# Kernel optimization log

Hardware: AMD Instinct MI355X
Metric: run time of the kernel (lower is better)

## Reference

```python
import jax, jax.numpy as jnp
import numpy as np
import math

B, S, E, H, DFF = 4, 1024, 1024, 16, 4096
HD = E // H
EPS = 1e-8


def setup_inputs() -> dict:
    key = jax.random.key(0)
    ks = jax.random.split(key, 16)
    sc = 0.02
    inp = {
        'x': jax.random.normal(ks[0], (B, S, E), jnp.float32),
        'mask': jax.random.randint(ks[1], (B, S, S), 0, 2, jnp.int32),
        'Wq': jax.random.normal(ks[2], (E, E), jnp.float32) * sc,
        'bq': jnp.zeros((E,), jnp.float32),
        'Wk': jax.random.normal(ks[3], (E, E), jnp.float32) * sc,
        'bk': jnp.zeros((E,), jnp.float32),
        'Wv': jax.random.normal(ks[4], (E, E), jnp.float32) * sc,
        'bv': jnp.zeros((E,), jnp.float32),
        'Wo': jax.random.normal(ks[5], (E, E), jnp.float32) * sc,
        'bo': jnp.zeros((E,), jnp.float32),
        'W1': jax.random.normal(ks[6], (DFF, E), jnp.float32) * sc,
        'b1': jnp.zeros((DFF,), jnp.float32),
        'W2': jax.random.normal(ks[7], (E, DFF), jnp.float32) * sc,
        'b2': jnp.zeros((E,), jnp.float32),
        'g1': jnp.ones((E,), jnp.float32),
        'be1': jnp.zeros((E,), jnp.float32),
        'g2': jnp.ones((E,), jnp.float32),
        'be2': jnp.zeros((E,), jnp.float32),
    }
    return inp


def _layernorm(x, g, b):
    # torch LayerNorm here: (x-mean)/(std+eps), std is unbiased (ddof=1)
    mean = jnp.mean(x, axis=-1, keepdims=True)
    std = jnp.std(x, axis=-1, keepdims=True, ddof=1)
    return g * (x - mean) / (std + EPS) + b


def _gelu(x):
    c = math.sqrt(2.0 / math.pi)
    return 0.5 * x * (1.0 + jnp.tanh(c * (x + 0.044715 * x ** 3)))


def _block(x, mask_f, Wq, bq, Wk, bk, Wv, bv, Wo, bo, W1, b1, W2, b2, g1, be1, g2, be2):
    # --- attention sublayer (pre-norm, residual) ---
    nx = _layernorm(x, g1, be1)
    q = (nx @ Wq.T + bq).reshape(B, S, H, HD).transpose(0, 2, 1, 3)  # [B,H,S,D]
    k = (nx @ Wk.T + bk).reshape(B, S, H, HD).transpose(0, 2, 1, 3)
    v = (nx @ Wv.T + bv).reshape(B, S, H, HD).transpose(0, 2, 1, 3)
    scores = jnp.einsum('bhqd,bhkd->bhqk', q, k) / math.sqrt(HD)
    m = mask_f[:, None, :, :]  # [B,1,S,S]
    scores = jnp.where(m == 0, jnp.float32(-0.01), scores * m)
    p = jax.nn.softmax(scores, axis=-1)
    o = jnp.einsum('bhqk,bhkd->bhqd', p, v)  # [B,H,S,D]
    o = o.transpose(0, 2, 1, 3).reshape(B, S, E)
    x = x + (o @ Wo.T + bo)
    # --- FFN sublayer ---
    nx2 = _layernorm(x, g2, be2)
    ff = _gelu(nx2 @ W1.T + b1) @ W2.T + b2
    return x + ff


def reference(x, mask, Wq, bq, Wk, bk, Wv, bv, Wo, bo, W1, b1, W2, b2, g1, be1, g2, be2):
    mask_f = mask.astype(jnp.float32)
    return _block(x, mask_f, Wq, bq, Wk, bk, Wv, bv, Wo, bo, W1, b1, W2, b2, g1, be1, g2, be2)
```

## Files before the change

### kernel.cpp

```cpp
#include <hip/hip_runtime.h>
#include <math.h>

typedef __attribute__((ext_vector_type(8))) short short8;
typedef __attribute__((ext_vector_type(4))) float f32x4;
typedef __attribute__((ext_vector_type(4))) int   i32x4v;

#define B_   4
#define S_   1024
#define E_   1024
#define H_   16
#define DFF_ 4096

#define HB_MAX 4.0f

__device__ __forceinline__ ushort f2bf(float f){
  unsigned int x = __float_as_uint(f);
  x += 0x7fffu + ((x >> 16) & 1u);
  return (ushort)(x >> 16);
}

__device__ __forceinline__ unsigned int pk_bf16_trunc(float a, float b){
  return __builtin_amdgcn_perm(__float_as_uint(b), __float_as_uint(a), 0x07060302u);
}

__device__ __forceinline__ float gelu_f(float x){
  const float c = 0.7978845608028654f;
  float u = 2.0f * c * (x + 0.044715f * x * x * x);
  return x / (1.0f + __expf(-u));
}

__device__ __forceinline__ void gl2lds16(const void* g, void* l){
  __builtin_amdgcn_global_load_lds(
      (const __attribute__((address_space(1))) void*)g,
      (__attribute__((address_space(3))) void*)l, 16, 0, 0);
}

__device__ __forceinline__ int q8(float x, float s){
  float v = fmaxf(fminf(x * s, 127.f), -127.f);
  return ((int)__builtin_rintf(v)) & 255;
}
__device__ __forceinline__ int pk_i8x4(float a, float b, float c, float d, float s){
  return q8(a,s) | (q8(b,s) << 8) | (q8(c,s) << 16) | (q8(d,s) << 24);
}

__global__ __launch_bounds__(256) void prep_kernel(
    const float* __restrict__ Wq, const float* __restrict__ Wk,
    const float* __restrict__ Wv, const float* __restrict__ Wo,
    const float* __restrict__ W1, const float* __restrict__ W2,
    const float* __restrict__ bq, const float* __restrict__ bk,
    const float* __restrict__ bv, const int* __restrict__ mask,
    unsigned char* __restrict__ bQKV8, float* __restrict__ sQKV,
    unsigned char* __restrict__ bWo8, float* __restrict__ sWo,
    unsigned char* __restrict__ bW18, float* __restrict__ sW1,
    unsigned char* __restrict__ bW28, float* __restrict__ sW2,
    float* __restrict__ cbias, unsigned long long* __restrict__ maskp)
{
  int blk = blockIdx.x, t = threadIdx.x;
  __shared__ float sm[4];

  if (blk < 4096){
    float4 v = ((const float4*)(W1 + (size_t)blk * 1024))[t];
    float m = fmaxf(fmaxf(fabsf(v.x), fabsf(v.y)), fmaxf(fabsf(v.z), fabsf(v.w)));
    #pragma unroll
    for (int o = 32; o; o >>= 1) m = fmaxf(m, __shfl_xor(m, o));
    if ((t & 63) == 0) sm[t >> 6] = m;
    __syncthreads();
    float mx = fmaxf(fmaxf(sm[0], sm[1]), fmaxf(sm[2], sm[3])) + 1e-20f;
    float qs = 127.0f / mx;
    ((int*)(bW18 + (size_t)blk * 1024))[t] = pk_i8x4(v.x, v.y, v.z, v.w, qs);
    if (t == 0) sW1[blk] = mx * (1.0f / 127.0f);
    return;
  }
  if (blk < 5120){
    int r = blk - 4096;
    float4 v[4]; float m = 0.f;
    #pragma unroll
    for (int i = 0; i < 4; i++){
      v[i] = ((const float4*)(W2 + (size_t)r * 4096))[t + i * 256];
      m = fmaxf(m, fmaxf(fmaxf(fabsf(v[i].x), fabsf(v[i].y)), fmaxf(fabsf(v[i].z), fabsf(v[i].w))));
    }
    #pragma unroll
    for (int o = 32; o; o >>= 1) m = fmaxf(m, __shfl_xor(m, o));
    if ((t & 63) == 0) sm[t >> 6] = m;
    __syncthreads();
    float mx = fmaxf(fmaxf(sm[0], sm[1]), fmaxf(sm[2], sm[3])) + 1e-20f;
    float qs = 127.0f / mx;
    #pragma unroll
    for (int i = 0; i < 4; i++)
      ((int*)(bW28 + (size_t)r * 4096))[t + i * 256] = pk_i8x4(v[i].x, v[i].y, v[i].z, v[i].w, qs);
    if (t == 0) sW2[r] = mx * (1.0f / 127.0f);
    return;
  }
  if (blk < 8192){
    int r = blk - 5120;
    const float* src = (r < 1024) ? Wq + (size_t)r * 1024
                     : (r < 2048) ? Wk + (size_t)(r - 1024) * 1024
                                  : Wv + (size_t)(r - 2048) * 1024;
    float4 v = ((const float4*)src)[t];
    float m = fmaxf(fmaxf(fabsf(v.x), fabsf(v.y)), fmaxf(fabsf(v.z), fabsf(v.w)));
    #pragma unroll
    for (int o = 32; o; o >>= 1) m = fmaxf(m, __shfl_xor(m, o));
    if ((t & 63) == 0) sm[t >> 6] = m;
    __syncthreads();
    float mx = fmaxf(fmaxf(sm[0], sm[1]), fmaxf(sm[2], sm[3])) + 1e-20f;
    float qs = 127.0f / mx;
    ((int*)(bQKV8 + (size_t)r * 1024))[t] = pk_i8x4(v.x, v.y, v.z, v.w, qs);
    if (t == 0) sQKV[r] = mx * (1.0f / 127.0f);
    return;
  }
  if (blk < 9216){
    int r = blk - 8192;
    float4 v = ((const float4*)(Wo + (size_t)r * 1024))[t];
    float m = fmaxf(fmaxf(fabsf(v.x), fabsf(v.y)), fmaxf(fabsf(v.z), fabsf(v.w)));
    #pragma unroll
    for (int o = 32; o; o >>= 1) m = fmaxf(m, __shfl_xor(m, o));
    if ((t & 63) == 0) sm[t >> 6] = m;
    __syncthreads();
    float mx = fmaxf(fmaxf(sm[0], sm[1]), fmaxf(sm[2], sm[3])) + 1e-20f;
    float qs = 127.0f / mx;
    ((int*)(bWo8 + (size_t)r * 1024))[t] = pk_i8x4(v.x, v.y, v.z, v.w, qs);
    if (t == 0) sWo[r] = mx * (1.0f / 127.0f);
    return;
  }
  if (blk == 9216){
    #pragma unroll
    for (int r = 0; r < 12; r++){
      int idx = r * 256 + t;
      cbias[idx] = (idx < 1024) ? bq[idx] : (idx < 2048 ? bk[idx - 1024] : bv[idx - 2048]);
    }
    return;
  }
  int widx = (blk - 9217) * 4 + (t >> 6);
  int mv = mask[(size_t)widx * 64 + (t & 63)];
  unsigned long long bal = __ballot(mv != 0);
  if ((t & 63) == 0) maskp[widx] = bal;
}

__global__ __launch_bounds__(256) void ln_i8(const float* __restrict__ x,
    const float* __restrict__ g, const float* __restrict__ be,
    unsigned char* __restrict__ out8, float* __restrict__ sOut){
  int row = blockIdx.x, t = threadIdx.x;
  float4 v = ((const float4*)(x + (size_t)row * E_))[t];
  float s = v.x + v.y + v.z + v.w;
  float q = v.x*v.x + v.y*v.y + v.z*v.z + v.w*v.w;
  #pragma unroll
  for (int o = 32; o; o >>= 1){ s += __shfl_xor(s, o); q += __shfl_xor(q, o); }
  __shared__ float ss[4], sq[4], sm[4];
  int w = t >> 6;
  if ((t & 63) == 0){ ss[w] = s; sq[w] = q; }
  __syncthreads();
  s = ss[0] + ss[1] + ss[2] + ss[3];
  q = sq[0] + sq[1] + sq[2] + sq[3];
  float mean = s * (1.0f / E_);
  float var  = fmaxf((q - (float)E_ * mean * mean) * (1.0f / (E_ - 1)), 0.0f);
  float inv = 1.0f / (sqrtf(var) + 1e-8f);
  float4 gv = ((const float4*)g)[t];
  float4 bv = ((const float4*)be)[t];
  float n0 = gv.x * (v.x - mean) * inv + bv.x;
  float n1 = gv.y * (v.y - mean) * inv + bv.y;
  float n2 = gv.z * (v.z - mean) * inv + bv.z;
  float n3 = gv.w * (v.w - mean) * inv + bv.w;
  float m = fmaxf(fmaxf(fabsf(n0), fabsf(n1)), fmaxf(fabsf(n2), fabsf(n3)));
  #pragma unroll
  for (int o = 32; o; o >>= 1) m = fmaxf(m, __shfl_xor(m, o));
  if ((t & 63) == 0) sm[w] = m;
  __syncthreads();
  float mx = fmaxf(fmaxf(sm[0], sm[1]), fmaxf(sm[2], sm[3])) + 1e-20f;
  float qs = 127.0f / mx;
  ((int*)(out8 + (size_t)row * E_))[t] = pk_i8x4(n0, n1, n2, n3, qs);
  if (t == 0) sOut[row] = mx * (1.0f / 127.0f);
}

__global__ __launch_bounds__(256) void ln2_fuse(const float* __restrict__ x,
    const float* __restrict__ P, const float* __restrict__ bo,
    const float* __restrict__ g, const float* __restrict__ be,
    float* __restrict__ x2, unsigned char* __restrict__ nx28, float* __restrict__ sOut){
  int row = blockIdx.x, t = threadIdx.x;
  size_t idx = (size_t)row * 256 + t;
  float4 v  = ((const float4*)x)[idx];
  float4 p0 = ((const float4*)P)[idx];
  float4 p1 = ((const float4*)P)[idx + 1048576];
  float4 bv0 = ((const float4*)bo)[t];
  v.x += p0.x + p1.x + bv0.x;
  v.y += p0.y + p1.y + bv0.y;
  v.z += p0.z + p1.z + bv0.z;
  v.w += p0.w + p1.w + bv0.w;
  ((float4*)x2)[idx] = v;
  float s = v.x + v.y + v.z + v.w;
  float q = v.x*v.x + v.y*v.y + v.z*v.z + v.w*v.w;
  #pragma unroll
  for (int o = 32; o; o >>= 1){ s += __shfl_xor(s, o); q += __shfl_xor(q, o); }
  __shared__ float ss[4], sq[4], sm[4];
  int w = t >> 6;
  if ((t & 63) == 0){ ss[w] = s; sq[w] = q; }
  __syncthreads();
  s = ss[0] + ss[1] + ss[2] + ss[3];
  q = sq[0] + sq[1] + sq[2] + sq[3];
  float mean = s * (1.0f / E_);
  float var  = fmaxf((q - (float)E_ * mean * mean) * (1.0f / (E_ - 1)), 0.0f);
  float inv = 1.0f / (sqrtf(var) + 1e-8f);
  float4 gv = ((const float4*)g)[t];
  float4 bev = ((const float4*)be)[t];
  float n0 = gv.x * (v.x - mean) * inv + bev.x;
  float n1 = gv.y * (v.y - mean) * inv + bev.y;
  float n2 = gv.z * (v.z - mean) * inv + bev.z;
  float n3 = gv.w * (v.w - mean) * inv + bev.w;
  float m = fmaxf(fmaxf(fabsf(n0), fabsf(n1)), fmaxf(fabsf(n2), fabsf(n3)));
  #pragma unroll
  for (int o = 32; o; o >>= 1) m = fmaxf(m, __shfl_xor(m, o));
  if ((t & 63) == 0) sm[w] = m;
  __syncthreads();
  float mx = fmaxf(fmaxf(sm[0], sm[1]), fmaxf(sm[2], sm[3])) + 1e-20f;
  float qs = 127.0f / mx;
  ((int*)(nx28 + (size_t)row * E_))[t] = pk_i8x4(n0, n1, n2, n3, qs);
  if (t == 0) sOut[row] = mx * (1.0f / 127.0f);
}

__global__ __launch_bounds__(256) void reduce_out(const float* __restrict__ x2,
    const float* __restrict__ P, const float* __restrict__ b2, float* __restrict__ out){
  size_t i = (size_t)blockIdx.x * 256 + threadIdx.x;
  int col4 = i & 255;
  float4 v  = ((const float4*)x2)[i];
  float4 p0 = ((const float4*)P)[i];
  float4 p1 = ((const float4*)P)[i + 1048576];
  float4 bv = ((const float4*)b2)[col4];
  float4 o;
  o.x = v.x + p0.x + p1.x + bv.x;
  o.y = v.y + p0.y + p1.y + bv.y;
  o.z = v.z + p0.z + p1.z + bv.z;
  o.w = v.w + p0.w + p1.w + bv.w;
  ((float4*)out)[i] = o;
}

template<int MODE>
__global__ __launch_bounds__(256) void gemm_i8(
    const unsigned char* __restrict__ A8, const unsigned char* __restrict__ B8,
    const float* __restrict__ sA, const float* __restrict__ sB,
    const float* __restrict__ bias,
    ushort* __restrict__ Cb, unsigned char* __restrict__ C8, float* __restrict__ Pf,
    int K, int ldc)
{
  __shared__ __align__(16) unsigned char As[128 * 128];
  __shared__ __align__(16) unsigned char Bs[128 * 128];
  const int t = threadIdx.x, w = t >> 6, ln = t & 63;
  const int quad = ln >> 4, lc = ln & 15;
  const int wm = w >> 1, wn = w & 1;
  const int m0 = blockIdx.y * 128, n0 = blockIdx.x * 128;
  int kbeg = 0, kend = K;
  if (MODE == 2){
    int kh = K >> 1;
    kbeg = blockIdx.z * kh; kend = kbeg + kh;
    Pf += (size_t)blockIdx.z * (4096 * 1024);
  }

  i32x4v acc[4][4];
  #pragma unroll
  for (int i = 0; i < 4; i++)
    #pragma unroll
    for (int j = 0; j < 4; j++) acc[i][j] = i32x4v{0, 0, 0, 0};

  for (int k0 = kbeg; k0 < kend; k0 += 128){
    __syncthreads();
    #pragma unroll
    for (int r2 = 0; r2 < 4; r2++){
      int chunk = r2 * 256 + t;
      int row = chunk >> 3;
      int co = ((chunk & 7) ^ (row & 7)) * 16;
      gl2lds16(A8 + (size_t)(m0 + row) * K + k0 + co, As + (size_t)(r2*256 + (t & 192)) * 16);
      gl2lds16(B8 + (size_t)(n0 + row) * K + k0 + co, Bs + (size_t)(r2*256 + (t & 192)) * 16);
    }
    __syncthreads();
    #pragma unroll
    for (int kk = 0; kk < 128; kk += 64){
      const int cb = kk >> 4;
      i32x4v af[4], bfr[4];
      #pragma unroll
      for (int i = 0; i < 4; i++){
        int row = wm*64 + i*16 + lc;
        af[i]  = *(const i32x4v*)(As + (size_t)row * 128 + (((cb + quad) ^ (row & 7)) * 16));
      }
      #pragma unroll
      for (int j = 0; j < 4; j++){
        int row = wn*64 + j*16 + lc;
        bfr[j] = *(const i32x4v*)(Bs + (size_t)row * 128 + (((cb + quad) ^ (row & 7)) * 16));
      }
      #pragma unroll
      for (int i = 0; i < 4; i++)
        #pragma unroll
        for (int j = 0; j < 4; j++)
          acc[i][j] = __builtin_amdgcn_mfma_i32_16x16x64_i8(af[i], bfr[j], acc[i][j], 0, 0, 0);
    }
  }

  #pragma unroll
  for (int j = 0; j < 4; j++){
    int col = n0 + wn*64 + j*16 + lc;
    float sb = sB[col];
    float bc = (MODE == 2) ? 0.f : bias[col];
    #pragma unroll
    for (int i = 0; i < 4; i++){
      int row0 = m0 + wm*64 + i*16 + quad*4;
      #pragma unroll
      for (int r = 0; r < 4; r++){
        int row = row0 + r;
        if (MODE == 0){
          float v = (float)acc[i][j][r] * sA[row] * sb + bc;
          float sc = (col < 1024) ? 0.125f : 1.0f;
          Cb[(size_t)row * ldc + col] = f2bf(v * sc);
        } else if (MODE == 1){
          float v = gelu_f((float)acc[i][j][r] * sA[row] * sb + bc);
          C8[(size_t)row * 4096 + col] = (unsigned char)q8(v, 127.0f / HB_MAX);
        } else {
          Pf[(size_t)row * 1024 + col] = (float)acc[i][j][r] * (HB_MAX / 127.0f) * sb;
        }
      }
    }
  }
}

__global__ __launch_bounds__(256) void vT_kernel(const ushort* __restrict__ QKV,
                                                 ushort* __restrict__ Vt){
  __shared__ ushort tile[64][68];
  int st = blockIdx.x;
  int bh = blockIdx.y;
  int b = bh >> 4, h = bh & 15;
  int t = threadIdx.x;
  #pragma unroll
  for (int it = 0; it < 4; it++){
    int idx = it * 256 + t;
    int r = idx >> 4, c4 = (idx & 15) * 4;
    ushort4 v = *(const ushort4*)(QKV + ((size_t)(b*1024 + st*64 + r)) * 3072 + 2048 + h*64 + c4);
    *(ushort4*)(&tile[r][c4]) = v;
  }
  __syncthreads();
  #pragma unroll
  for (int it = 0; it < 4; it++){
    int idx = it * 256 + t;
    int d = idx >> 4, s4 = (idx & 15) * 4;
    ushort4 o;
    o.x = tile[s4+0][d]; o.y = tile[s4+1][d]; o.z = tile[s4+2][d]; o.w = tile[s4+3][d];
    *(ushort4*)(Vt + ((size_t)bh * 64 + d) * 1024 + st*64 + s4) = o;
  }
}

__global__ __launch_bounds__(256) void attn_kernel(
    const ushort* __restrict__ QKV, const ushort* __restrict__ Vt,
    const unsigned long long* __restrict__ maskp, unsigned char* __restrict__ O8)
{
  __shared__ __align__(16) ushort Ks[64 * 64];
  __shared__ __align__(16) ushort Vs[64 * 64];
  __shared__ __align__(16) ushort Ps[4][16 * 72];

  const int t = threadIdx.x, w = t >> 6, ln = t & 63;
  const int quad = ln >> 4, lc = ln & 15;
  const int bh = blockIdx.x, b = bh >> 4;
  const int q0 = blockIdx.y * 64;
  const int coff = (bh & 15) * 64;
  const size_t rb = (size_t)b * S_;

  const int myq = q0 + w*16 + lc;
  const ushort* qrow = QKV + (rb + myq) * 3072 + coff;
  short8 qf0 = *(const short8*)(qrow + quad*8);
  short8 qf1 = *(const short8*)(qrow + 32 + quad*8);
  const unsigned long long* mrow = maskp + (rb + myq) * 16;

  f32x4 of[4];
  #pragma unroll
  for (int gd = 0; gd < 4; gd++) of[gd] = f32x4{0.f, 0.f, 0.f, 0.f};
  float lsum = 0.0f;
  const float PM = 0.99004983f;

  for (int k0 = 0; k0 < S_; k0 += 64){
    __syncthreads();
    #pragma unroll
    for (int it = 0; it < 2; it++){
      int chunk = it * 256 + t;
      int row = chunk >> 3, blk = chunk & 7;
      int dst = row * 64 + ((blk ^ (row & 7)) * 8);
      *(short8*)(Ks + dst) = *(const short8*)(QKV + (rb + k0 + row) * 3072 + 1024 + coff + blk*8);
      *(short8*)(Vs + dst) = *(const short8*)(Vt + ((size_t)bh * 64 + row) * 1024 + k0 + blk*8);
    }
    unsigned long long m64 = mrow[k0 >> 6];
    __syncthreads();

    f32x4 sf[4];
    #pragma unroll
    for (int g = 0; g < 4; g++){
      int krow = g*16 + lc;
      short8 kf0 = *(const short8*)(Ks + krow*64 + ((quad       ^ (lc & 7)) * 8));
      short8 kf1 = *(const short8*)(Ks + krow*64 + (((4 + quad) ^ (lc & 7)) * 8));
      f32x4 z = f32x4{0.f, 0.f, 0.f, 0.f};
      z = __builtin_amdgcn_mfma_f32_16x16x32_bf16(kf0, qf0, z, 0, 0, 0);
      z = __builtin_amdgcn_mfma_f32_16x16x32_bf16(kf1, qf1, z, 0, 0, 0);
      sf[g] = z;
    }

    #pragma unroll
    for (int g = 0; g < 4; g++){
      unsigned int b4 = (unsigned int)(m64 >> (g*16 + quad*4)) & 0xFu;
      float p0 = (b4 & 1u) ? __expf(sf[g][0]) : PM;
      float p1 = (b4 & 2u) ? __expf(sf[g][1]) : PM;
      float p2 = (b4 & 4u) ? __expf(sf[g][2]) : PM;
      float p3 = (b4 & 8u) ? __expf(sf[g][3]) : PM;
      lsum += p0 + p1 + p2 + p3;
      uint2 pw;
      pw.x = pk_bf16_trunc(p0, p1);
      pw.y = pk_bf16_trunc(p2, p3);
      *(uint2*)(&Ps[w][lc*72 + g*16 + quad*4]) = pw;
    }

    short8 pf0 = *(const short8*)(&Ps[w][lc*72 + quad*8]);
    short8 pf1 = *(const short8*)(&Ps[w][lc*72 + 32 + quad*8]);
    #pragma unroll
    for (int gd = 0; gd < 4; gd++){
      int vrow = gd*16 + lc;
      short8 vf0 = *(const short8*)(Vs + vrow*64 + ((quad       ^ (lc & 7)) * 8));
      short8 vf1 = *(const short8*)(Vs + vrow*64 + (((4 + quad) ^ (lc & 7)) * 8));
      of[gd] = __builtin_amdgcn_mfma_f32_16x16x32_bf16(vf0, pf0, of[gd], 0, 0, 0);
      of[gd] = __builtin_amdgcn_mfma_f32_16x16x32_bf16(vf1, pf1, of[gd], 0, 0, 0);
    }
  }

  lsum += __shfl_xor(lsum, 16);
  lsum += __shfl_xor(lsum, 32);
  float inv = 1.0f / lsum;

  unsigned char* orow = O8 + (rb + myq) * E_ + coff;
  #pragma unroll
  for (int gd = 0; gd < 4; gd++){
    int pk = pk_i8x4(of[gd][0] * inv, of[gd][1] * inv,
                     of[gd][2] * inv, of[gd][3] * inv, 127.0f / HB_MAX);
    *(int*)(orow + gd*16 + quad*4) = pk;
  }
}

extern "C" void kernel_launch(void* const* d_in, const int* in_sizes, int n_in,
                              void* d_out, int out_size, void* d_ws, size_t ws_size,
                              hipStream_t stream)
{
  const float* x   = (const float*)d_in[0];
  const int*   mask= (const int*)  d_in[1];
  const float* Wq  = (const float*)d_in[2];
  const float* bq  = (const float*)d_in[3];
  const float* Wk  = (const float*)d_in[4];
  const float* bk  = (const float*)d_in[5];
  const float* Wv  = (const float*)d_in[6];
  const float* bv  = (const float*)d_in[7];
  const float* Wo  = (const float*)d_in[8];
  const float* bo  = (const float*)d_in[9];
  const float* W1  = (const float*)d_in[10];
  const float* b1  = (const float*)d_in[11];
  const float* W2  = (const float*)d_in[12];
  const float* b2  = (const float*)d_in[13];
  const float* g1  = (const float*)d_in[14];
  const float* be1 = (const float*)d_in[15];
  const float* g2  = (const float*)d_in[16];
  const float* be2 = (const float*)d_in[17];
  float* out = (float*)d_out;

  char* ws = (char*)d_ws;
  size_t off = 0;
  auto alloc = [&](size_t bytes) -> void* {
    void* p = ws + off; off += (bytes + 255) & ~(size_t)255; return p;
  };
  const size_t MM = 1024 * 1024;
  unsigned char* bQKV8 = (unsigned char*)alloc(3 * MM);
  float* sQKV  = (float*)alloc(3072 * 4);
  unsigned char* bWo8 = (unsigned char*)alloc(MM);
  float* sWo   = (float*)alloc(1024 * 4);
  unsigned char* bW18 = (unsigned char*)alloc(4 * MM);
  float* sW1   = (float*)alloc(4096 * 4);
  unsigned char* bW28 = (unsigned char*)alloc(4 * MM);
  float* sW2   = (float*)alloc(1024 * 4);
  float* cbias = (float*)alloc(3072 * 4);
  unsigned long long* maskp = (unsigned long long*)alloc(65536 * 8);
  unsigned char* nx8  = (unsigned char*)alloc(4 * MM);
  float* sX1   = (float*)alloc(4096 * 4);
  ushort* QKV  = (ushort*)alloc(12 * MM * 2);
  ushort* VtG  = (ushort*)alloc(4 * MM * 2);
  unsigned char* Ob8 = (unsigned char*)alloc(4 * MM);
  float*  x2   = (float*) alloc(4 * MM * 4);
  unsigned char* nx28 = (unsigned char*)alloc(4 * MM);
  float* sX2   = (float*)alloc(4096 * 4);
  unsigned char* hb8  = (unsigned char*)alloc(16 * MM);

  float* Pbuf = (float*)nx8;

  prep_kernel<<<25601, 256, 0, stream>>>(Wq, Wk, Wv, Wo, W1, W2, bq, bk, bv, mask,
                                         bQKV8, sQKV, bWo8, sWo, bW18, sW1, bW28, sW2,
                                         cbias, maskp);

  ln_i8<<<4096, 256, 0, stream>>>(x, g1, be1, nx8, sX1);

  gemm_i8<0><<<dim3(24, 32), 256, 0, stream>>>(
      nx8, bQKV8, sX1, sQKV, cbias, QKV, nullptr, nullptr, 1024, 3072);

  vT_kernel<<<dim3(16, 64), 256, 0, stream>>>(QKV, VtG);

  attn_kernel<<<dim3(64, 16), 256, 0, stream>>>(QKV, VtG, maskp, Ob8);

  gemm_i8<2><<<dim3(8, 32, 2), 256, 0, stream>>>(
      Ob8, bWo8, nullptr, sWo, nullptr, nullptr, nullptr, Pbuf, 1024, 1024);

  ln2_fuse<<<4096, 256, 0, stream>>>(x, Pbuf, bo, g2, be2, x2, nx28, sX2);

  gemm_i8<1><<<dim3(32, 32), 256, 0, stream>>>(
      nx28, bW18, sX2, sW1, b1, nullptr, hb8, nullptr, 1024, 4096);

  gemm_i8<2><<<dim3(8, 32, 2), 256, 0, stream>>>(
      hb8, bW28, nullptr, sW2, nullptr, nullptr, nullptr, Pbuf, 4096, 1024);

  reduce_out<<<4096, 256, 0, stream>>>(x2, Pbuf, b2, out);
}
```

Baseline: 320.2 us.

## Double-buffer attention K/V tiles with direct global-to-LDS loads; regroup prep per wavefront

```diff
diff --git a/kernel.cpp b/kernel.cpp
--- a/kernel.cpp
+++ b/kernel.cpp
@@ -56,73 +56,58 @@
     float* __restrict__ cbias, unsigned long long* __restrict__ maskp)
 {
   int blk = blockIdx.x, t = threadIdx.x;
-  __shared__ float sm[4];
-
-  if (blk < 4096){
-    float4 v = ((const float4*)(W1 + (size_t)blk * 1024))[t];
-    float m = fmaxf(fmaxf(fabsf(v.x), fabsf(v.y)), fmaxf(fabsf(v.z), fabsf(v.w)));
+  int w = t >> 6, ln = t & 63;
+
+  if (blk < 2048){
+    int row = blk * 4 + w;
+    const float* src; unsigned char* dst; float* sdst;
+    if (row < 1024){      src = Wq + (size_t)row * 1024;
+                          dst = bQKV8 + (size_t)row * 1024; sdst = sQKV + row; }
+    else if (row < 2048){ src = Wk + (size_t)(row - 1024) * 1024;
+                          dst = bQKV8 + (size_t)row * 1024; sdst = sQKV + row; }
+    else if (row < 3072){ src = Wv + (size_t)(row - 2048) * 1024;
+                          dst = bQKV8 + (size_t)row * 1024; sdst = sQKV + row; }
+    else if (row < 4096){ int r = row - 3072; src = Wo + (size_t)r * 1024;
+                          dst = bWo8 + (size_t)r * 1024; sdst = sWo + r; }
+    else                { int r = row - 4096; src = W1 + (size_t)r * 1024;
+                          dst = bW18 + (size_t)r * 1024; sdst = sW1 + r; }
+    float4 v[4]; float m = 0.f;
+    #pragma unroll
+    for (int i = 0; i < 4; i++){
+      v[i] = ((const float4*)src)[ln + i * 64];
+      m = fmaxf(m, fmaxf(fmaxf(fabsf(v[i].x), fabsf(v[i].y)),
+                         fmaxf(fabsf(v[i].z), fabsf(v[i].w))));
+    }
     #pragma unroll
     for (int o = 32; o; o >>= 1) m = fmaxf(m, __shfl_xor(m, o));
-    if ((t & 63) == 0) sm[t >> 6] = m;
-    __syncthreads();
-    float mx = fmaxf(fmaxf(sm[0], sm[1]), fmaxf(sm[2], sm[3])) + 1e-20f;
-    float qs = 127.0f / mx;
-    ((int*)(bW18 + (size_t)blk * 1024))[t] = pk_i8x4(v.x, v.y, v.z, v.w, qs);
-    if (t == 0) sW1[blk] = mx * (1.0f / 127.0f);
+    float mx = m + 1e-20f, qs = 127.0f / mx;
+    #pragma unroll
+    for (int i = 0; i < 4; i++)
+      ((int*)dst)[ln + i * 64] = pk_i8x4(v[i].x, v[i].y, v[i].z, v[i].w, qs);
+    if (ln == 0) *sdst = mx * (1.0f / 127.0f);
     return;
   }
-  if (blk < 5120){
-    int r = blk - 4096;
-    float4 v[4]; float m = 0.f;
-    #pragma unroll
-    for (int i = 0; i < 4; i++){
-      v[i] = ((const float4*)(W2 + (size_t)r * 4096))[t + i * 256];
-      m = fmaxf(m, fmaxf(fmaxf(fabsf(v[i].x), fabsf(v[i].y)), fmaxf(fabsf(v[i].z), fabsf(v[i].w))));
+  if (blk < 2304){
+    int r = (blk - 2048) * 4 + w;
+    const float* src = W2 + (size_t)r * 4096;
+    float4 v[16]; float m = 0.f;
+    #pragma unroll
+    for (int i = 0; i < 16; i++){
+      v[i] = ((const float4*)src)[ln + i * 64];
+      m = fmaxf(m, fmaxf(fmaxf(fabsf(v[i].x), fabsf(v[i].y)),
+                         fmaxf(fabsf(v[i].z), fabsf(v[i].w))));
     }
     #pragma unroll
     for (int o = 32; o; o >>= 1) m = fmaxf(m, __shfl_xor(m, o));
-    if ((t & 63) == 0) sm[t >> 6] = m;
-    __syncthreads();
-    float mx = fmaxf(fmaxf(sm[0], sm[1]), fmaxf(sm[2], sm[3])) + 1e-20f;
-    float qs = 127.0f / mx;
-    #pragma unroll
-    for (int i = 0; i < 4; i++)
-      ((int*)(bW28 + (size_t)r * 4096))[t + i * 256] = pk_i8x4(v[i].x, v[i].y, v[i].z, v[i].w, qs);
-    if (t == 0) sW2[r] = mx * (1.0f / 127.0f);
+    float mx = m + 1e-20f, qs = 127.0f / mx;
+    #pragma unroll
+    for (int i = 0; i < 16; i++)
+      ((int*)(bW28 + (size_t)r * 4096))[ln + i * 64] =
+          pk_i8x4(v[i].x, v[i].y, v[i].z, v[i].w, qs);
+    if (ln == 0) sW2[r] = mx * (1.0f / 127.0f);
     return;
   }
-  if (blk < 8192){
-    int r = blk - 5120;
-    const float* src = (r < 1024) ? Wq + (size_t)r * 1024
-                     : (r < 2048) ? Wk + (size_t)(r - 1024) * 1024
-                                  : Wv + (size_t)(r - 2048) * 1024;
-    float4 v = ((const float4*)src)[t];
-    float m = fmaxf(fmaxf(fabsf(v.x), fabsf(v.y)), fmaxf(fabsf(v.z), fabsf(v.w)));
-    #pragma unroll
-    for (int o = 32; o; o >>= 1) m = fmaxf(m, __shfl_xor(m, o));
-    if ((t & 63) == 0) sm[t >> 6] = m;
-    __syncthreads();
-    float mx = fmaxf(fmaxf(sm[0], sm[1]), fmaxf(sm[2], sm[3])) + 1e-20f;
-    float qs = 127.0f / mx;
-    ((int*)(bQKV8 + (size_t)r * 1024))[t] = pk_i8x4(v.x, v.y, v.z, v.w, qs);
-    if (t == 0) sQKV[r] = mx * (1.0f / 127.0f);
-    return;
-  }
-  if (blk < 9216){
-    int r = blk - 8192;
-    float4 v = ((const float4*)(Wo + (size_t)r * 1024))[t];
-    float m = fmaxf(fmaxf(fabsf(v.x), fabsf(v.y)), fmaxf(fabsf(v.z), fabsf(v.w)));
-    #pragma unroll
-    for (int o = 32; o; o >>= 1) m = fmaxf(m, __shfl_xor(m, o));
-    if ((t & 63) == 0) sm[t >> 6] = m;
-    __syncthreads();
-    float mx = fmaxf(fmaxf(sm[0], sm[1]), fmaxf(sm[2], sm[3])) + 1e-20f;
-    float qs = 127.0f / mx;
-    ((int*)(bWo8 + (size_t)r * 1024))[t] = pk_i8x4(v.x, v.y, v.z, v.w, qs);
-    if (t == 0) sWo[r] = mx * (1.0f / 127.0f);
-    return;
-  }
-  if (blk == 9216){
+  if (blk == 2304){
     #pragma unroll
     for (int r = 0; r < 12; r++){
       int idx = r * 256 + t;
@@ -130,10 +115,14 @@
     }
     return;
   }
-  int widx = (blk - 9217) * 4 + (t >> 6);
-  int mv = mask[(size_t)widx * 64 + (t & 63)];
-  unsigned long long bal = __ballot(mv != 0);
-  if ((t & 63) == 0) maskp[widx] = bal;
+  int wbase = (blk - 2305) * 16 + w * 4;
+  #pragma unroll
+  for (int j = 0; j < 4; j++){
+    int widx = wbase + j;
+    int mv = mask[(size_t)widx * 64 + ln];
+    unsigned long long bal = __ballot(mv != 0);
+    if (ln == 0) maskp[widx] = bal;
+  }
 }
 
 __global__ __launch_bounds__(256) void ln_i8(const float* __restrict__ x,
@@ -347,8 +336,8 @@
     const ushort* __restrict__ QKV, const ushort* __restrict__ Vt,
     const unsigned long long* __restrict__ maskp, unsigned char* __restrict__ O8)
 {
-  __shared__ __align__(16) ushort Ks[64 * 64];
-  __shared__ __align__(16) ushort Vs[64 * 64];
+  __shared__ __align__(16) ushort Ks[2][64 * 64];
+  __shared__ __align__(16) ushort Vs[2][64 * 64];
   __shared__ __align__(16) ushort Ps[4][16 * 72];
 
   const int t = threadIdx.x, w = t >> 6, ln = t & 63;
@@ -364,31 +353,41 @@
   short8 qf1 = *(const short8*)(qrow + 32 + quad*8);
   const unsigned long long* mrow = maskp + (rb + myq) * 16;
 
+  auto stage = [&](int kt, int buf){
+    int k0 = kt * 64;
+    #pragma unroll
+    for (int it = 0; it < 2; it++){
+      int chunk = it * 256 + t;
+      int row = chunk >> 3;
+      int co = ((chunk & 7) ^ (row & 7)) * 8;
+      gl2lds16(QKV + (rb + k0 + row) * 3072 + 1024 + coff + co,
+               Ks[buf] + (size_t)(it*256 + (t & 192)) * 8);
+      gl2lds16(Vt + ((size_t)bh * 64 + row) * 1024 + k0 + co,
+               Vs[buf] + (size_t)(it*256 + (t & 192)) * 8);
+    }
+  };
+
   f32x4 of[4];
   #pragma unroll
   for (int gd = 0; gd < 4; gd++) of[gd] = f32x4{0.f, 0.f, 0.f, 0.f};
   float lsum = 0.0f;
   const float PM = 0.99004983f;
 
-  for (int k0 = 0; k0 < S_; k0 += 64){
+  stage(0, 0);
+  for (int kt = 0; kt < 16; kt++){
+    int buf = kt & 1;
+    unsigned long long m64 = mrow[kt];
     __syncthreads();
-    #pragma unroll
-    for (int it = 0; it < 2; it++){
-      int chunk = it * 256 + t;
-      int row = chunk >> 3, blk = chunk & 7;
-      int dst = row * 64 + ((blk ^ (row & 7)) * 8);
-      *(short8*)(Ks + dst) = *(const short8*)(QKV + (rb + k0 + row) * 3072 + 1024 + coff + blk*8);
-      *(short8*)(Vs + dst) = *(const short8*)(Vt + ((size_t)bh * 64 + row) * 1024 + k0 + blk*8);
-    }
-    unsigned long long m64 = mrow[k0 >> 6];
-    __syncthreads();
+    if (kt < 15) stage(kt + 1, buf ^ 1);
+    const ushort* ks = Ks[buf];
+    const ushort* vs = Vs[buf];
 
     f32x4 sf[4];
     #pragma unroll
     for (int g = 0; g < 4; g++){
       int krow = g*16 + lc;
-      short8 kf0 = *(const short8*)(Ks + krow*64 + ((quad       ^ (lc & 7)) * 8));
-      short8 kf1 = *(const short8*)(Ks + krow*64 + (((4 + quad) ^ (lc & 7)) * 8));
+      short8 kf0 = *(const short8*)(ks + krow*64 + ((quad       ^ (lc & 7)) * 8));
+      short8 kf1 = *(const short8*)(ks + krow*64 + (((4 + quad) ^ (lc & 7)) * 8));
       f32x4 z = f32x4{0.f, 0.f, 0.f, 0.f};
       z = __builtin_amdgcn_mfma_f32_16x16x32_bf16(kf0, qf0, z, 0, 0, 0);
       z = __builtin_amdgcn_mfma_f32_16x16x32_bf16(kf1, qf1, z, 0, 0, 0);
@@ -414,8 +413,8 @@
     #pragma unroll
     for (int gd = 0; gd < 4; gd++){
       int vrow = gd*16 + lc;
-      short8 vf0 = *(const short8*)(Vs + vrow*64 + ((quad       ^ (lc & 7)) * 8));
-      short8 vf1 = *(const short8*)(Vs + vrow*64 + (((4 + quad) ^ (lc & 7)) * 8));
+      short8 vf0 = *(const short8*)(vs + vrow*64 + ((quad       ^ (lc & 7)) * 8));
+      short8 vf1 = *(const short8*)(vs + vrow*64 + (((4 + quad) ^ (lc & 7)) * 8));
       of[gd] = __builtin_amdgcn_mfma_f32_16x16x32_bf16(vf0, pf0, of[gd], 0, 0, 0);
       of[gd] = __builtin_amdgcn_mfma_f32_16x16x32_bf16(vf1, pf1, of[gd], 0, 0, 0);
     }
@@ -486,9 +485,9 @@
 
   float* Pbuf = (float*)nx8;
 
-  prep_kernel<<<25601, 256, 0, stream>>>(Wq, Wk, Wv, Wo, W1, W2, bq, bk, bv, mask,
-                                         bQKV8, sQKV, bWo8, sWo, bW18, sW1, bW28, sW2,
-                                         cbias, maskp);
+  prep_kernel<<<6401, 256, 0, stream>>>(Wq, Wk, Wv, Wo, W1, W2, bq, bk, bv, mask,
+                                        bQKV8, sQKV, bWo8, sWo, bW18, sW1, bW28, sW2,
+                                        cbias, maskp);
 
   ln_i8<<<4096, 256, 0, stream>>>(x, g1, be1, nx8, sX1);
 
```

New measurement: 317.6 us. Within noise of the previous version (-0.8%).
